# Optimization experiments

Measured on AMD Instinct MI355X. Metric: run time of the kernel, lower is better.

## Reference

```python
import jax, jax.numpy as jnp
import numpy as np

S, B, D, H, K, M, MEM = 1024, 2, 1024, 16, 64, 4096, 1
T = (MEM + 1) * S  # key length = (mem_len+1)*seq_len


def setup_inputs() -> dict:
    key = jax.random.key(0)
    ks = jax.random.split(key, 16)

    def w(k, shape):  # N(0, 0.02) init as in the torch module
        return jax.random.normal(k, shape, dtype=jnp.float32) * 0.02

    x = jax.random.normal(ks[0], (S, B, D), dtype=jnp.float32)
    p = jax.random.normal(ks[1], (T, B, D), dtype=jnp.float32)
    memory = jax.random.normal(ks[2], (MEM * S, B, D), dtype=jnp.float32)
    u_bias = w(ks[3], (H, K))
    v_bias = w(ks[4], (H, K))
    # Transformer-XL causal mask: query s may attend to keys t <= mem_len*S + s
    t_idx = jnp.arange(T)[None, :]
    s_idx = jnp.arange(S)[:, None]
    mask = jnp.where(t_idx <= MEM * S + s_idx, 0.0, -1e9).astype(jnp.float32)[None]  # [1,S,T]
    return {
        "x": x, "p": p, "mask": mask, "memory": memory,
        "u_bias": u_bias, "v_bias": v_bias,
        "wq_w": w(ks[5], (H * K, D)), "wke_w": w(ks[6], (H * K, D)),
        "wkr_w": w(ks[7], (H * K, D)), "wv_w": w(ks[8], (H * K, D)),
        "wc_w": w(ks[9], (D, H * K)),
        "w1_w": w(ks[10], (M, D)), "w1_b": jnp.zeros((M,), jnp.float32),
        "w2_w": w(ks[11], (D, M)), "w2_b": jnp.zeros((D,), jnp.float32),
        "ln1_g": jnp.ones((D,), jnp.float32), "ln1_b": jnp.zeros((D,), jnp.float32),
        "ln2_g": jnp.ones((D,), jnp.float32), "ln2_b": jnp.zeros((D,), jnp.float32),
    }


def _layernorm(x, g, b, eps=1e-5):
    mu = jnp.mean(x, axis=-1, keepdims=True)
    var = jnp.mean(jnp.square(x - mu), axis=-1, keepdims=True)
    return (x - mu) / jnp.sqrt(var + eps) * g + b


def reference(x, p, mask, memory, u_bias, v_bias,
              wq_w, wke_w, wkr_w, wv_w, wc_w,
              w1_w, w1_b, w2_w, w2_b, ln1_g, ln1_b, ln2_g, ln2_b):
    s_len, b_sz, d = x.shape
    q = (x @ wq_w.T).reshape(s_len, b_sz, H, K)            # [S,B,H,K]
    x_mem = jnp.concatenate([memory, x], axis=0)           # [T,B,D]
    k_e = (x_mem @ wke_w.T).reshape(T, b_sz, H, K)         # content keys
    k_r = (p @ wkr_w.T).reshape(T, b_sz, H, K)             # relative-position keys
    v = (x_mem @ wv_w.T).reshape(T, b_sz, H, K)
    # AC: content score, BD: relative-position score (Transformer-XL)
    ac = jnp.einsum("sbhk,tbhk->bhst", q + u_bias, k_e)
    bd = jnp.einsum("sbhk,tbhk->bhst", q + v_bias, k_r)
    alpha = (ac + bd) / np.sqrt(K).astype(np.float32) + mask[:, None]  # [B,H,S,T]
    alpha = jax.nn.softmax(alpha, axis=-1)
    av = jnp.einsum("bhst,tbhk->sbhk", alpha, v).reshape(s_len, b_sz, H * K)
    u = av @ wc_w.T
    u = _layernorm(u + x, ln1_g, ln1_b)
    z = jax.nn.relu(u @ w1_w.T + w1_b) @ w2_w.T + w2_b
    z = _layernorm(z + u, ln2_g, ln2_b)
    return z
```

## Files before the change

### kernel.cpp

```cpp
#include <hip/hip_runtime.h>
#include <math.h>

#define S_LEN 1024
#define BATCH 2
#define DM 1024
#define NH 16
#define HD 64
#define FFN_DIM 4096
#define T_LEN 2048
#define RQ 2048
#define RT 4096
#define KROW 72
#define NPART 2

typedef __attribute__((ext_vector_type(8))) short short8;
typedef __attribute__((ext_vector_type(4))) float f32x4;

__device__ __forceinline__ unsigned short f2bf(float f) {
    unsigned u = __builtin_bit_cast(unsigned, f);
    u += 0x7fffu + ((u >> 16) & 1u);
    return (unsigned short)(u >> 16);
}
__device__ __forceinline__ float bf2f(unsigned short s) { return __builtin_bit_cast(float, ((unsigned)s) << 16); }

#define GLD_LDS16(gptr, lptr)                                                                  \
    __builtin_amdgcn_global_load_lds((const __attribute__((address_space(1))) unsigned int*)(gptr), \
                                     (__attribute__((address_space(3))) unsigned int*)(lptr), 16, 0, 0)

__device__ __forceinline__ ushort4 cvt4(float4 v) {
    ushort4 o;
    o.x = f2bf(v.x); o.y = f2bf(v.y); o.z = f2bf(v.z); o.w = f2bf(v.w);
    return o;
}

__global__ void cast_all_kernel(const float* __restrict__ wq, const float* __restrict__ wke,
                                const float* __restrict__ wv, const float* __restrict__ wkr,
                                const float* __restrict__ wc, const float* __restrict__ w1,
                                const float* __restrict__ w2, const float* __restrict__ x,
                                const float* __restrict__ p, const float* __restrict__ mem,
                                unsigned short* __restrict__ wdst, unsigned short* __restrict__ xbf,
                                unsigned short* __restrict__ pbf, unsigned short* __restrict__ xm) {
    const long Q = 256 * 1024;
    const long W = 13 * Q;
    long i = (long)blockIdx.x * blockDim.x + threadIdx.x;
    if (i < W) {
        const float* src; long off;
        if      (i < 1 * Q) { src = wq;  off = 0; }
        else if (i < 2 * Q) { src = wke; off = 1 * Q; }
        else if (i < 3 * Q) { src = wv;  off = 2 * Q; }
        else if (i < 4 * Q) { src = wkr; off = 3 * Q; }
        else if (i < 5 * Q) { src = wc;  off = 4 * Q; }
        else if (i < 9 * Q) { src = w1;  off = 5 * Q; }
        else                { src = w2;  off = 9 * Q; }
        ((ushort4*)wdst)[i] = cvt4(((const float4*)src)[i - off]);
    } else if (i < W + 2 * Q) {
        long j = i - W;
        ((ushort4*)xbf)[j] = cvt4(((const float4*)x)[j]);
    } else if (i < W + 6 * Q) {
        long j = i - W - 2 * Q;
        ((ushort4*)pbf)[j] = cvt4(((const float4*)p)[j]);
    } else {
        long j = i - W - 6 * Q;
        float4 v = (j < 2 * Q) ? ((const float4*)mem)[j] : ((const float4*)x)[j - 2 * Q];
        ((ushort4*)xm)[j] = cvt4(v);
    }
}

#define BM 128
#define BN 64
#define BK 32

__launch_bounds__(256)
__global__ void proj_fused(const unsigned short* __restrict__ xbf, const unsigned short* __restrict__ xmbf,
                           const unsigned short* __restrict__ pbf, const unsigned short* __restrict__ wqb,
                           const unsigned short* __restrict__ wkevb, const unsigned short* __restrict__ wkrb,
                           unsigned short* __restrict__ qo, unsigned short* __restrict__ keo,
                           unsigned short* __restrict__ vTo, unsigned short* __restrict__ kro) {
    __shared__ __align__(16) short As[BM * BK];
    __shared__ __align__(16) short Bs[BN * BK];
    const int id = blockIdx.x;
    const unsigned short *A, *B;
    unsigned short *Yb, *Yv = nullptr;
    int bx, by;
    if (id < 256)       { A = xbf;  B = wqb;   Yb = qo;  bx = id & 15;  by = id >> 4; }
    else if (id < 1280) { int t = id - 256;  A = xmbf; B = wkevb; Yb = keo; Yv = vTo;
                          bx = t & 31; by = t >> 5; }
    else                { int t = id - 1280; A = pbf;  B = wkrb;  Yb = kro;
                          bx = t & 15; by = t >> 4; }
    const int tid = threadIdx.x;
    const int w = tid >> 6, lane = tid & 63;
    const int row0 = by * BM, col0 = bx * BN;
    const int wr = (w >> 1) * 64, wcn = (w & 1) * 32;
    f32x4 acc[4][2] = {};
    const int lrow = lane & 15, quad = lane >> 4;
    for (int k0 = 0; k0 < DM; k0 += BK) {
        __syncthreads();
#pragma unroll
        for (int i = 0; i < 2; ++i) {
            int c = w * 128 + i * 64 + lane;
            int row = c >> 2, kg = c & 3;
            int kl = (kg - (row >> 1)) & 3;
            GLD_LDS16(A + (long)(row0 + row) * DM + k0 + kl * 8, As + (w * 128 + i * 64) * 8);
        }
        {
            int row = tid >> 2, kg = tid & 3;
            int kl = (kg - (row >> 1)) & 3;
            GLD_LDS16(B + (long)(col0 + row) * DM + k0 + kl * 8, Bs + (w * 64) * 8);
        }
        __syncthreads();
        short8 a[4], b[2];
#pragma unroll
        for (int mi = 0; mi < 4; ++mi) {
            int r = wr + mi * 16 + lrow;
            int ph = (quad + (r >> 1)) & 3;
            a[mi] = *(const short8*)&As[r * BK + ph * 8];
        }
#pragma unroll
        for (int ni = 0; ni < 2; ++ni) {
            int r = wcn + ni * 16 + lrow;
            int ph = (quad + (r >> 1)) & 3;
            b[ni] = *(const short8*)&Bs[r * BK + ph * 8];
        }
#pragma unroll
        for (int mi = 0; mi < 4; ++mi)
#pragma unroll
            for (int ni = 0; ni < 2; ++ni)
                acc[mi][ni] = __builtin_amdgcn_mfma_f32_16x16x32_bf16(a[mi], b[ni], acc[mi][ni], 0, 0, 0);
    }
    const int mb = row0 + wr + quad * 4;
    const int nb = col0 + wcn + lrow;
    const bool iske = (col0 < 1024);
#pragma unroll
    for (int mi = 0; mi < 4; ++mi)
#pragma unroll
        for (int ni = 0; ni < 2; ++ni) {
            const int r = mb + mi * 16, cc = nb + ni * 16;
#pragma unroll
            for (int reg = 0; reg < 4; ++reg) {
                float val = acc[mi][ni][reg];
                const int rf = r + reg;
                if (Yv && !iske) {
                    int c2 = cc - 1024;
                    int t = rf >> 1, b2 = rf & 1;
                    int h2 = c2 >> 6, d2 = c2 & 63;
                    Yv[((long)(b2 * NH + h2) * HD + d2) * T_LEN + t] = f2bf(val);
                } else {
                    Yb[(long)rf * DM + cc] = f2bf(val);
                }
            }
        }
}

__launch_bounds__(256)
__global__ void gemm_mfma(const unsigned short* __restrict__ A, const unsigned short* __restrict__ B,
                          const float* __restrict__ bias, float* __restrict__ Yf,
                          unsigned short* __restrict__ Yb, int Kd, int N, int relu) {
    __shared__ __align__(16) short As[BM * BK];
    __shared__ __align__(16) short Bs[BN * BK];
    const int tid = threadIdx.x;
    const int w = tid >> 6, lane = tid & 63;
    const int row0 = blockIdx.y * BM, col0 = blockIdx.x * BN;
    const int wr = (w >> 1) * 64, wcn = (w & 1) * 32;
    f32x4 acc[4][2] = {};
    const int lrow = lane & 15, quad = lane >> 4;
    for (int k0 = 0; k0 < Kd; k0 += BK) {
        __syncthreads();
#pragma unroll
        for (int i = 0; i < 2; ++i) {
            int c = w * 128 + i * 64 + lane;
            int row = c >> 2, kg = c & 3;
            int kl = (kg - (row >> 1)) & 3;
            GLD_LDS16(A + (long)(row0 + row) * Kd + k0 + kl * 8, As + (w * 128 + i * 64) * 8);
        }
        {
            int row = tid >> 2, kg = tid & 3;
            int kl = (kg - (row >> 1)) & 3;
            GLD_LDS16(B + (long)(col0 + row) * Kd + k0 + kl * 8, Bs + (w * 64) * 8);
        }
        __syncthreads();
        short8 a[4], b[2];
#pragma unroll
        for (int mi = 0; mi < 4; ++mi) {
            int r = wr + mi * 16 + lrow;
            int ph = (quad + (r >> 1)) & 3;
            a[mi] = *(const short8*)&As[r * BK + ph * 8];
        }
#pragma unroll
        for (int ni = 0; ni < 2; ++ni) {
            int r = wcn + ni * 16 + lrow;
            int ph = (quad + (r >> 1)) & 3;
            b[ni] = *(const short8*)&Bs[r * BK + ph * 8];
        }
#pragma unroll
        for (int mi = 0; mi < 4; ++mi)
#pragma unroll
            for (int ni = 0; ni < 2; ++ni)
                acc[mi][ni] = __builtin_amdgcn_mfma_f32_16x16x32_bf16(a[mi], b[ni], acc[mi][ni], 0, 0, 0);
    }
    const int mb = row0 + wr + quad * 4;
    const int nb = col0 + wcn + lrow;
    float bb[2];
#pragma unroll
    for (int ni = 0; ni < 2; ++ni) bb[ni] = bias ? bias[nb + ni * 16] : 0.f;
#pragma unroll
    for (int mi = 0; mi < 4; ++mi)
#pragma unroll
        for (int ni = 0; ni < 2; ++ni) {
            const int r = mb + mi * 16, cc = nb + ni * 16;
#pragma unroll
            for (int reg = 0; reg < 4; ++reg) {
                float val = acc[mi][ni][reg] + bb[ni];
                if (relu) val = fmaxf(val, 0.f);
                if (Yb) Yb[(long)(r + reg) * N + cc] = f2bf(val);
                else    Yf[(long)(r + reg) * N + cc] = val;
            }
        }
}

__launch_bounds__(256)
__global__ void prep_kernel(const unsigned short* __restrict__ kr,
                            const float* __restrict__ ub, const float* __restrict__ vb,
                            unsigned short* __restrict__ ke_io, float* __restrict__ biasg) {
    const int r = blockIdx.x;
    const int tid = threadIdx.x;
    const int h = tid >> 4, seg = tid & 15;
    ushort4 keu = ((const ushort4*)(ke_io + (long)r * DM))[tid];
    ushort4 kru = ((const ushort4*)(kr + (long)r * DM))[tid];
    float ke0 = bf2f(keu.x), ke1 = bf2f(keu.y), ke2 = bf2f(keu.z), ke3 = bf2f(keu.w);
    float kr0 = bf2f(kru.x), kr1 = bf2f(kru.y), kr2 = bf2f(kru.z), kr3 = bf2f(kru.w);
    float4 u4 = ((const float4*)ub)[tid];
    float4 v4 = ((const float4*)vb)[tid];
    ushort4 s;
    s.x = f2bf((ke0 + kr0) * 0.125f); s.y = f2bf((ke1 + kr1) * 0.125f);
    s.z = f2bf((ke2 + kr2) * 0.125f); s.w = f2bf((ke3 + kr3) * 0.125f);
    ((ushort4*)(ke_io + (long)r * DM))[tid] = s;
    float part = u4.x * ke0 + u4.y * ke1 + u4.z * ke2 + u4.w * ke3
               + v4.x * kr0 + v4.y * kr1 + v4.z * kr2 + v4.w * kr3;
    part += __shfl_xor(part, 1);
    part += __shfl_xor(part, 2);
    part += __shfl_xor(part, 4);
    part += __shfl_xor(part, 8);
    if (seg == 0) {
        const int t = r >> 1, b = r & 1;
        biasg[(b * NH + h) * T_LEN + t] = part * 0.125f;
    }
}

__launch_bounds__(256)
__global__ void attn_mfma(const unsigned short* __restrict__ qg,
                          const unsigned short* __restrict__ ksum,
                          const unsigned short* __restrict__ vT,
                          const float* __restrict__ biasg,
                          float* __restrict__ Opart, float2* __restrict__ mlout) {
    __shared__ __align__(16) unsigned short Ks[64 * KROW];
    __shared__ __align__(16) unsigned short Vs[64 * KROW];
    __shared__ __align__(16) unsigned short Ps[4][16 * KROW];
    const int bid = blockIdx.x;
    const int part = bid >> 9, rid = bid & 511;
    const int stile = rid & 15, h = (rid >> 4) & 15, b = rid >> 8;
    const int tid = threadIdx.x, w = tid >> 6, lane = tid & 63;
    const int L = lane & 15, quad = lane >> 4;
    const int qbase = stile * 64 + w * 16;
    short8 qf0, qf1;
    {
        const unsigned short* qp = qg + ((long)(qbase + L) * 2 + b) * DM + h * HD + quad * 8;
        qf0 = *(const short8*)(qp);
        qf1 = *(const short8*)(qp + 32);
    }
    f32x4 O[4] = {};
    float mrow[4] = {-1e30f, -1e30f, -1e30f, -1e30f};
    float lrow[4] = {0.f, 0.f, 0.f, 0.f};
    const int nch = 17 + stile;
    const float* bias_p = biasg + (long)(b * NH + h) * T_LEN;
    const unsigned short* ks_base = ksum + (long)b * DM + h * HD;
    const unsigned short* vt_base = vT + (long)(b * NH + h) * HD * T_LEN;
    const int c0 = tid, c1 = 256 + tid;
    const int row_a = c0 >> 3, seg_a = c0 & 7;
    const int row_b = c1 >> 3, seg_b = c1 & 7;
    uint4 pk0, pk1, pv0, pv1;
    {
        const int tf = part * 64;
        pk0 = *(const uint4*)(ks_base + (long)(tf + row_a) * 2 * DM + seg_a * 8);
        pk1 = *(const uint4*)(ks_base + (long)(tf + row_b) * 2 * DM + seg_b * 8);
        pv0 = *(const uint4*)(vt_base + (long)row_a * T_LEN + tf + seg_a * 8);
        pv1 = *(const uint4*)(vt_base + (long)row_b * T_LEN + tf + seg_b * 8);
    }
    for (int ch = part; ch < nch; ch += NPART) {
        const int t0 = ch * 64;
        __syncthreads();
        *(uint4*)&Ks[row_a * KROW + seg_a * 8] = pk0;
        *(uint4*)&Ks[row_b * KROW + seg_b * 8] = pk1;
        *(uint4*)&Vs[row_a * KROW + seg_a * 8] = pv0;
        *(uint4*)&Vs[row_b * KROW + seg_b * 8] = pv1;
        __syncthreads();
        if (ch + NPART < nch) {
            const int t1 = t0 + NPART * 64;
            pk0 = *(const uint4*)(ks_base + (long)(t1 + row_a) * 2 * DM + seg_a * 8);
            pk1 = *(const uint4*)(ks_base + (long)(t1 + row_b) * 2 * DM + seg_b * 8);
            pv0 = *(const uint4*)(vt_base + (long)row_a * T_LEN + t1 + seg_a * 8);
            pv1 = *(const uint4*)(vt_base + (long)row_b * T_LEN + t1 + seg_b * 8);
        }
        f32x4 S[4] = {};
#pragma unroll
        for (int kt = 0; kt < 4; ++kt) {
            short8 kb0 = *(const short8*)&Ks[(kt * 16 + L) * KROW + quad * 8];
            short8 kb1 = *(const short8*)&Ks[(kt * 16 + L) * KROW + 32 + quad * 8];
            S[kt] = __builtin_amdgcn_mfma_f32_16x16x32_bf16(qf0, kb0, S[kt], 0, 0, 0);
            S[kt] = __builtin_amdgcn_mfma_f32_16x16x32_bf16(qf1, kb1, S[kt], 0, 0, 0);
        }
        float sc[4][4];
        float cm[4] = {-1e30f, -1e30f, -1e30f, -1e30f};
#pragma unroll
        for (int kt = 0; kt < 4; ++kt) {
            float bt = bias_p[t0 + kt * 16 + L];
#pragma unroll
            for (int reg = 0; reg < 4; ++reg) {
                float v = S[kt][reg] + bt;
                if (t0 + kt * 16 + L > 1024 + qbase + quad * 4 + reg) v = -1e30f;
                sc[kt][reg] = v;
                cm[reg] = fmaxf(cm[reg], v);
            }
        }
#pragma unroll
        for (int off = 1; off < 16; off <<= 1)
#pragma unroll
            for (int reg = 0; reg < 4; ++reg) cm[reg] = fmaxf(cm[reg], __shfl_xor(cm[reg], off));
        float cf[4];
#pragma unroll
        for (int reg = 0; reg < 4; ++reg) {
            float mn = fmaxf(mrow[reg], cm[reg]);
            cf[reg] = __expf(mrow[reg] - mn);
            mrow[reg] = mn;
            lrow[reg] *= cf[reg];
        }
        float rs[4] = {0.f, 0.f, 0.f, 0.f};
#pragma unroll
        for (int kt = 0; kt < 4; ++kt)
#pragma unroll
            for (int reg = 0; reg < 4; ++reg) {
                float pv = __expf(sc[kt][reg] - mrow[reg]);
                rs[reg] += pv;
                Ps[w][(quad * 4 + reg) * KROW + kt * 16 + L] = f2bf(pv);
            }
#pragma unroll
        for (int off = 1; off < 16; off <<= 1)
#pragma unroll
            for (int reg = 0; reg < 4; ++reg) rs[reg] += __shfl_xor(rs[reg], off);
#pragma unroll
        for (int reg = 0; reg < 4; ++reg) lrow[reg] += rs[reg];
#pragma unroll
        for (int dt = 0; dt < 4; ++dt)
#pragma unroll
            for (int reg = 0; reg < 4; ++reg) O[dt][reg] *= cf[reg];
        short8 pa0 = *(const short8*)&Ps[w][L * KROW + quad * 8];
        short8 pa1 = *(const short8*)&Ps[w][L * KROW + 32 + quad * 8];
#pragma unroll
        for (int dt = 0; dt < 4; ++dt) {
            short8 vb0 = *(const short8*)&Vs[(dt * 16 + L) * KROW + quad * 8];
            short8 vb1 = *(const short8*)&Vs[(dt * 16 + L) * KROW + 32 + quad * 8];
            O[dt] = __builtin_amdgcn_mfma_f32_16x16x32_bf16(pa0, vb0, O[dt], 0, 0, 0);
            O[dt] = __builtin_amdgcn_mfma_f32_16x16x32_bf16(pa1, vb1, O[dt], 0, 0, 0);
        }
    }
    const long rbase = ((long)(part * 2 + b) * NH + h) * S_LEN;
#pragma unroll
    for (int reg = 0; reg < 4; ++reg) {
        const int s = qbase + quad * 4 + reg;
        float* op = Opart + (rbase + s) * 64;
#pragma unroll
        for (int dt = 0; dt < 4; ++dt) op[dt * 16 + L] = O[dt][reg];
        if (L == 0) mlout[rbase + s] = make_float2(mrow[reg], lrow[reg]);
    }
}

__launch_bounds__(256)
__global__ void attn_combine(const float* __restrict__ Opart, const float2* __restrict__ ml,
                             unsigned short* __restrict__ avout) {
    const int i = blockIdx.x * 256 + threadIdx.x;
    const int d4 = i & 15;
    const int row = i >> 4;
    const int s = row & 1023;
    const int bh = row >> 10;
    const int b = bh >> 4, h = bh & 15;
    float2 ml0 = ml[row], ml1 = ml[row + 32768];
    float m = fmaxf(ml0.x, ml1.x);
    float a0 = __expf(ml0.x - m), a1 = __expf(ml1.x - m);
    float inv = 1.f / (a0 * ml0.y + a1 * ml1.y);
    a0 *= inv; a1 *= inv;
    float4 o0 = ((const float4*)Opart)[(long)row * 16 + d4];
    float4 o1 = ((const float4*)Opart)[((long)row + 32768) * 16 + d4];
    float4 o;
    o.x = a0 * o0.x + a1 * o1.x;
    o.y = a0 * o0.y + a1 * o1.y;
    o.z = a0 * o0.z + a1 * o1.z;
    o.w = a0 * o0.w + a1 * o1.w;
    *(ushort4*)(avout + ((long)s * 2 + b) * DM + h * HD + d4 * 4) = cvt4(o);
}

__launch_bounds__(256)
__global__ void ln_kernel(const float* __restrict__ a, const float* __restrict__ r,
                          const float* __restrict__ g, const float* __restrict__ be,
                          float* __restrict__ out, unsigned short* __restrict__ outb) {
    const int row = blockIdx.x;
    const int tid = threadIdx.x;
    float4 xa = ((const float4*)(a + (long)row * DM))[tid];
    float4 xr = ((const float4*)(r + (long)row * DM))[tid];
    float4 x = make_float4(xa.x + xr.x, xa.y + xr.y, xa.z + xr.z, xa.w + xr.w);
    float s1 = x.x + x.y + x.z + x.w;
    float s2 = x.x * x.x + x.y * x.y + x.z * x.z + x.w * x.w;
#pragma unroll
    for (int off = 32; off > 0; off >>= 1) {
        s1 += __shfl_down(s1, off);
        s2 += __shfl_down(s2, off);
    }
    __shared__ float w1s[4], w2s[4];
    const int wid = tid >> 6;
    if ((tid & 63) == 0) { w1s[wid] = s1; w2s[wid] = s2; }
    __syncthreads();
    float S1 = w1s[0] + w1s[1] + w1s[2] + w1s[3];
    float S2 = w2s[0] + w2s[1] + w2s[2] + w2s[3];
    float mu = S1 * (1.f / 1024.f);
    float var = S2 * (1.f / 1024.f) - mu * mu;
    float rstd = rsqrtf(var + 1e-5f);
    float4 gv = ((const float4*)g)[tid];
    float4 bv = ((const float4*)be)[tid];
    float4 o;
    o.x = (x.x - mu) * rstd * gv.x + bv.x;
    o.y = (x.y - mu) * rstd * gv.y + bv.y;
    o.z = (x.z - mu) * rstd * gv.z + bv.z;
    o.w = (x.w - mu) * rstd * gv.w + bv.w;
    ((float4*)(out + (long)row * DM))[tid] = o;
    if (outb) ((ushort4*)(outb + (long)row * DM))[tid] = cvt4(o);
}

extern "C" void kernel_launch(void* const* d_in, const int* in_sizes, int n_in,
                              void* d_out, int out_size, void* d_ws, size_t ws_size,
                              hipStream_t stream) {
    (void)in_sizes; (void)n_in; (void)out_size; (void)ws_size;
    const float* x    = (const float*)d_in[0];
    const float* p    = (const float*)d_in[1];
    const float* mem  = (const float*)d_in[3];
    const float* ub   = (const float*)d_in[4];
    const float* vb   = (const float*)d_in[5];
    const float* wq   = (const float*)d_in[6];
    const float* wke  = (const float*)d_in[7];
    const float* wkr  = (const float*)d_in[8];
    const float* wv   = (const float*)d_in[9];
    const float* wc   = (const float*)d_in[10];
    const float* w1   = (const float*)d_in[11];
    const float* w1b  = (const float*)d_in[12];
    const float* w2   = (const float*)d_in[13];
    const float* w2b  = (const float*)d_in[14];
    const float* ln1g = (const float*)d_in[15];
    const float* ln1b = (const float*)d_in[16];
    const float* ln2g = (const float*)d_in[17];
    const float* ln2b = (const float*)d_in[18];
    float* out = (float*)d_out;
    float* wsf = (float*)d_ws;
    unsigned short* ws16 = (unsigned short*)d_ws;

    const long HLF = 512 * 1024;
    const long M16 = 1024 * 1024;
    unsigned short* wq_bf   = ws16 + 0 * M16;
    unsigned short* wkev_bf = ws16 + 1 * M16;
    unsigned short* wkr_bf  = ws16 + 3 * M16;
    unsigned short* wc_bf   = ws16 + 4 * M16;
    unsigned short* w1_bf   = ws16 + 5 * M16;
    unsigned short* w2_bf   = ws16 + 9 * M16;
    unsigned short* x_bf   = (unsigned short*)(wsf + 13 * HLF);
    unsigned short* xm_bf  = (unsigned short*)(wsf + 15 * HLF);
    unsigned short* p_bf   = (unsigned short*)(wsf + 19 * HLF);
    unsigned short* q_bf   = (unsigned short*)(wsf + 23 * HLF);
    unsigned short* ke_bf  = (unsigned short*)(wsf + 25 * HLF);
    unsigned short* kr_bf  = (unsigned short*)(wsf + 29 * HLF);
    unsigned short* vT_bf  = (unsigned short*)(wsf + 33 * HLF);
    float* abias           = wsf + 37 * HLF;
    float* Opart           = wsf + 15 * HLF;
    float2* mlpart         = (float2*)(wsf + 29 * HLF);
    unsigned short* avb_bf = (unsigned short*)(wsf + 13 * HLF);
    float* t1              = wsf + 29 * HLF;
    float* u               = wsf + 25 * HLF;
    unsigned short* u_bf   = (unsigned short*)(wsf + 23 * HLF);
    unsigned short* z1_bf  = (unsigned short*)(wsf + 15 * HLF);
    float* t2              = wsf + 29 * HLF;

    cast_all_kernel<<<23552, 256, 0, stream>>>(wq, wke, wv, wkr, wc, w1, w2, x, p, mem,
                                               ws16, x_bf, p_bf, xm_bf);
    proj_fused<<<1792, 256, 0, stream>>>(x_bf, xm_bf, p_bf, wq_bf, wkev_bf, wkr_bf,
                                         q_bf, ke_bf, vT_bf, kr_bf);
    prep_kernel<<<RT, 256, 0, stream>>>(kr_bf, ub, vb, ke_bf, abias);
    attn_mfma<<<512 * NPART, 256, 0, stream>>>(q_bf, ke_bf, vT_bf, abias, Opart, mlpart);
    attn_combine<<<2048, 256, 0, stream>>>(Opart, mlpart, avb_bf);
    gemm_mfma<<<dim3(16, 16), 256, 0, stream>>>(avb_bf, wc_bf, nullptr, t1, nullptr, DM, DM, 0);
    ln_kernel<<<RQ, 256, 0, stream>>>(t1, x, ln1g, ln1b, u, u_bf);
    gemm_mfma<<<dim3(64, 16), 256, 0, stream>>>(u_bf, w1_bf, w1b, nullptr, z1_bf, DM, FFN_DIM, 1);
    gemm_mfma<<<dim3(16, 16), 256, 0, stream>>>(z1_bf, w2_bf, w2b, t2, nullptr, FFN_DIM, DM, 0);
    ln_kernel<<<RQ, 256, 0, stream>>>(t2, u, ln2g, ln2b, out, nullptr);
}
```

Measured before the change: 425.2 us.

## Widen GEMM tiles to 128x128 and add split-K with partial sums reduced in layernorm

Doubles the N-tile of the projection and MLP GEMMs to 128, so each wave computes a 64x64 sub-tile and gets more MFMA work per shared-memory load. To keep the N=1024 GEMMs (output projection, second FFN) filling the GPU with the larger tiles, they are split along K into two partial outputs. The layernorm kernel sums the two partials and adds the deferred bias. This trades more register pressure and an extra fp32 partial-sum write and read for better operand reuse.

Measured after the change: 406.8 us. 1.05x faster.

```diff
diff --git a/kernel.cpp b/kernel.cpp
--- a/kernel.cpp
+++ b/kernel.cpp
@@ -67,7 +67,7 @@
 }
 
 #define BM 128
-#define BN 64
+#define BN 128
 #define BK 32
 
 __launch_bounds__(256)
@@ -82,16 +82,16 @@
     const unsigned short *A, *B;
     unsigned short *Yb, *Yv = nullptr;
     int bx, by;
-    if (id < 256)       { A = xbf;  B = wqb;   Yb = qo;  bx = id & 15;  by = id >> 4; }
-    else if (id < 1280) { int t = id - 256;  A = xmbf; B = wkevb; Yb = keo; Yv = vTo;
-                          bx = t & 31; by = t >> 5; }
-    else                { int t = id - 1280; A = pbf;  B = wkrb;  Yb = kro;
-                          bx = t & 15; by = t >> 4; }
+    if (id < 128)      { A = xbf;  B = wqb;   Yb = qo;  bx = id & 7;   by = id >> 3; }
+    else if (id < 640) { int t = id - 128; A = xmbf; B = wkevb; Yb = keo; Yv = vTo;
+                         bx = t & 15; by = t >> 4; }
+    else               { int t = id - 640; A = pbf;  B = wkrb;  Yb = kro;
+                         bx = t & 7;  by = t >> 3; }
     const int tid = threadIdx.x;
     const int w = tid >> 6, lane = tid & 63;
     const int row0 = by * BM, col0 = bx * BN;
-    const int wr = (w >> 1) * 64, wcn = (w & 1) * 32;
-    f32x4 acc[4][2] = {};
+    const int wr = (w >> 1) * 64, wcn = (w & 1) * 64;
+    f32x4 acc[4][4] = {};
     const int lrow = lane & 15, quad = lane >> 4;
     for (int k0 = 0; k0 < DM; k0 += BK) {
         __syncthreads();
@@ -101,14 +101,10 @@
             int row = c >> 2, kg = c & 3;
             int kl = (kg - (row >> 1)) & 3;
             GLD_LDS16(A + (long)(row0 + row) * DM + k0 + kl * 8, As + (w * 128 + i * 64) * 8);
-        }
-        {
-            int row = tid >> 2, kg = tid & 3;
-            int kl = (kg - (row >> 1)) & 3;
-            GLD_LDS16(B + (long)(col0 + row) * DM + k0 + kl * 8, Bs + (w * 64) * 8);
+            GLD_LDS16(B + (long)(col0 + row) * DM + k0 + kl * 8, Bs + (w * 128 + i * 64) * 8);
         }
         __syncthreads();
-        short8 a[4], b[2];
+        short8 a[4], b[4];
 #pragma unroll
         for (int mi = 0; mi < 4; ++mi) {
             int r = wr + mi * 16 + lrow;
@@ -116,7 +112,7 @@
             a[mi] = *(const short8*)&As[r * BK + ph * 8];
         }
 #pragma unroll
-        for (int ni = 0; ni < 2; ++ni) {
+        for (int ni = 0; ni < 4; ++ni) {
             int r = wcn + ni * 16 + lrow;
             int ph = (quad + (r >> 1)) & 3;
             b[ni] = *(const short8*)&Bs[r * BK + ph * 8];
@@ -124,22 +120,22 @@
 #pragma unroll
         for (int mi = 0; mi < 4; ++mi)
 #pragma unroll
-            for (int ni = 0; ni < 2; ++ni)
+            for (int ni = 0; ni < 4; ++ni)
                 acc[mi][ni] = __builtin_amdgcn_mfma_f32_16x16x32_bf16(a[mi], b[ni], acc[mi][ni], 0, 0, 0);
     }
     const int mb = row0 + wr + quad * 4;
     const int nb = col0 + wcn + lrow;
-    const bool iske = (col0 < 1024);
+    const bool isv = (Yv != nullptr) && (col0 >= 1024);
 #pragma unroll
     for (int mi = 0; mi < 4; ++mi)
 #pragma unroll
-        for (int ni = 0; ni < 2; ++ni) {
+        for (int ni = 0; ni < 4; ++ni) {
             const int r = mb + mi * 16, cc = nb + ni * 16;
 #pragma unroll
             for (int reg = 0; reg < 4; ++reg) {
                 float val = acc[mi][ni][reg];
                 const int rf = r + reg;
-                if (Yv && !iske) {
+                if (isv) {
                     int c2 = cc - 1024;
                     int t = rf >> 1, b2 = rf & 1;
                     int h2 = c2 >> 6, d2 = c2 & 63;
@@ -154,16 +150,18 @@
 __launch_bounds__(256)
 __global__ void gemm_mfma(const unsigned short* __restrict__ A, const unsigned short* __restrict__ B,
                           const float* __restrict__ bias, float* __restrict__ Yf,
-                          unsigned short* __restrict__ Yb, int Kd, int N, int relu) {
+                          unsigned short* __restrict__ Yb, int Kd, int N, int relu,
+                          int klen, long pstride) {
     __shared__ __align__(16) short As[BM * BK];
     __shared__ __align__(16) short Bs[BN * BK];
     const int tid = threadIdx.x;
     const int w = tid >> 6, lane = tid & 63;
     const int row0 = blockIdx.y * BM, col0 = blockIdx.x * BN;
-    const int wr = (w >> 1) * 64, wcn = (w & 1) * 32;
-    f32x4 acc[4][2] = {};
+    const int kbeg = blockIdx.z * klen;
+    const int wr = (w >> 1) * 64, wcn = (w & 1) * 64;
+    f32x4 acc[4][4] = {};
     const int lrow = lane & 15, quad = lane >> 4;
-    for (int k0 = 0; k0 < Kd; k0 += BK) {
+    for (int k0 = kbeg; k0 < kbeg + klen; k0 += BK) {
         __syncthreads();
 #pragma unroll
         for (int i = 0; i < 2; ++i) {
@@ -171,14 +169,10 @@
             int row = c >> 2, kg = c & 3;
             int kl = (kg - (row >> 1)) & 3;
             GLD_LDS16(A + (long)(row0 + row) * Kd + k0 + kl * 8, As + (w * 128 + i * 64) * 8);
-        }
-        {
-            int row = tid >> 2, kg = tid & 3;
-            int kl = (kg - (row >> 1)) & 3;
-            GLD_LDS16(B + (long)(col0 + row) * Kd + k0 + kl * 8, Bs + (w * 64) * 8);
+            GLD_LDS16(B + (long)(col0 + row) * Kd + k0 + kl * 8, Bs + (w * 128 + i * 64) * 8);
         }
         __syncthreads();
-        short8 a[4], b[2];
+        short8 a[4], b[4];
 #pragma unroll
         for (int mi = 0; mi < 4; ++mi) {
             int r = wr + mi * 16 + lrow;
@@ -186,7 +180,7 @@
             a[mi] = *(const short8*)&As[r * BK + ph * 8];
         }
 #pragma unroll
-        for (int ni = 0; ni < 2; ++ni) {
+        for (int ni = 0; ni < 4; ++ni) {
             int r = wcn + ni * 16 + lrow;
             int ph = (quad + (r >> 1)) & 3;
             b[ni] = *(const short8*)&Bs[r * BK + ph * 8];
@@ -194,25 +188,26 @@
 #pragma unroll
         for (int mi = 0; mi < 4; ++mi)
 #pragma unroll
-            for (int ni = 0; ni < 2; ++ni)
+            for (int ni = 0; ni < 4; ++ni)
                 acc[mi][ni] = __builtin_amdgcn_mfma_f32_16x16x32_bf16(a[mi], b[ni], acc[mi][ni], 0, 0, 0);
     }
     const int mb = row0 + wr + quad * 4;
     const int nb = col0 + wcn + lrow;
-    float bb[2];
-#pragma unroll
-    for (int ni = 0; ni < 2; ++ni) bb[ni] = bias ? bias[nb + ni * 16] : 0.f;
+    float* of = Yf ? Yf + (long)blockIdx.z * pstride : nullptr;
+    float bb[4];
+#pragma unroll
+    for (int ni = 0; ni < 4; ++ni) bb[ni] = bias ? bias[nb + ni * 16] : 0.f;
 #pragma unroll
     for (int mi = 0; mi < 4; ++mi)
 #pragma unroll
-        for (int ni = 0; ni < 2; ++ni) {
+        for (int ni = 0; ni < 4; ++ni) {
             const int r = mb + mi * 16, cc = nb + ni * 16;
 #pragma unroll
             for (int reg = 0; reg < 4; ++reg) {
                 float val = acc[mi][ni][reg] + bb[ni];
                 if (relu) val = fmaxf(val, 0.f);
                 if (Yb) Yb[(long)(r + reg) * N + cc] = f2bf(val);
-                else    Yf[(long)(r + reg) * N + cc] = val;
+                else    of[(long)(r + reg) * N + cc] = val;
             }
         }
 }
@@ -398,12 +393,21 @@
 }
 
 __launch_bounds__(256)
-__global__ void ln_kernel(const float* __restrict__ a, const float* __restrict__ r,
+__global__ void ln_kernel(const float* __restrict__ a0, const float* __restrict__ a1,
+                          const float* __restrict__ cb, const float* __restrict__ r,
                           const float* __restrict__ g, const float* __restrict__ be,
                           float* __restrict__ out, unsigned short* __restrict__ outb) {
     const int row = blockIdx.x;
     const int tid = threadIdx.x;
-    float4 xa = ((const float4*)(a + (long)row * DM))[tid];
+    float4 xa = ((const float4*)(a0 + (long)row * DM))[tid];
+    if (a1) {
+        float4 x1 = ((const float4*)(a1 + (long)row * DM))[tid];
+        xa.x += x1.x; xa.y += x1.y; xa.z += x1.z; xa.w += x1.w;
+    }
+    if (cb) {
+        float4 c4 = ((const float4*)cb)[tid];
+        xa.x += c4.x; xa.y += c4.y; xa.z += c4.z; xa.w += c4.w;
+    }
     float4 xr = ((const float4*)(r + (long)row * DM))[tid];
     float4 x = make_float4(xa.x + xr.x, xa.y + xr.y, xa.z + xr.z, xa.w + xr.w);
     float s1 = x.x + x.y + x.z + x.w;
@@ -478,22 +482,26 @@
     float* Opart           = wsf + 15 * HLF;
     float2* mlpart         = (float2*)(wsf + 29 * HLF);
     unsigned short* avb_bf = (unsigned short*)(wsf + 13 * HLF);
-    float* t1              = wsf + 29 * HLF;
+    float* t1p             = wsf + 15 * HLF;
     float* u               = wsf + 25 * HLF;
     unsigned short* u_bf   = (unsigned short*)(wsf + 23 * HLF);
     unsigned short* z1_bf  = (unsigned short*)(wsf + 15 * HLF);
-    float* t2              = wsf + 29 * HLF;
+    float* t2p             = wsf + 29 * HLF;
+    const long PSTR = (long)2048 * 1024;
 
     cast_all_kernel<<<23552, 256, 0, stream>>>(wq, wke, wv, wkr, wc, w1, w2, x, p, mem,
                                                ws16, x_bf, p_bf, xm_bf);
-    proj_fused<<<1792, 256, 0, stream>>>(x_bf, xm_bf, p_bf, wq_bf, wkev_bf, wkr_bf,
-                                         q_bf, ke_bf, vT_bf, kr_bf);
+    proj_fused<<<896, 256, 0, stream>>>(x_bf, xm_bf, p_bf, wq_bf, wkev_bf, wkr_bf,
+                                        q_bf, ke_bf, vT_bf, kr_bf);
     prep_kernel<<<RT, 256, 0, stream>>>(kr_bf, ub, vb, ke_bf, abias);
     attn_mfma<<<512 * NPART, 256, 0, stream>>>(q_bf, ke_bf, vT_bf, abias, Opart, mlpart);
     attn_combine<<<2048, 256, 0, stream>>>(Opart, mlpart, avb_bf);
-    gemm_mfma<<<dim3(16, 16), 256, 0, stream>>>(avb_bf, wc_bf, nullptr, t1, nullptr, DM, DM, 0);
-    ln_kernel<<<RQ, 256, 0, stream>>>(t1, x, ln1g, ln1b, u, u_bf);
-    gemm_mfma<<<dim3(64, 16), 256, 0, stream>>>(u_bf, w1_bf, w1b, nullptr, z1_bf, DM, FFN_DIM, 1);
-    gemm_mfma<<<dim3(16, 16), 256, 0, stream>>>(z1_bf, w2_bf, w2b, t2, nullptr, FFN_DIM, DM, 0);
-    ln_kernel<<<RQ, 256, 0, stream>>>(t2, u, ln2g, ln2b, out, nullptr);
-}
+    gemm_mfma<<<dim3(8, 16, 2), 256, 0, stream>>>(avb_bf, wc_bf, nullptr, t1p, nullptr,
+                                                  DM, DM, 0, 512, PSTR);
+    ln_kernel<<<RQ, 256, 0, stream>>>(t1p, t1p + PSTR, nullptr, x, ln1g, ln1b, u, u_bf);
+    gemm_mfma<<<dim3(32, 16, 1), 256, 0, stream>>>(u_bf, w1_bf, w1b, nullptr, z1_bf,
+                                                   DM, FFN_DIM, 1, DM, 0);
+    gemm_mfma<<<dim3(8, 16, 2), 256, 0, stream>>>(z1_bf, w2_bf, nullptr, t2p, nullptr,
+                                                  FFN_DIM, DM, 0, 2048, PSTR);
+    ln_kernel<<<RQ, 256, 0, stream>>>(t2p, t2p + PSTR, w2b, u, ln2g, ln2b, out, nullptr);
+}
```
